# Performance work log

Hardware: AMD Instinct MI355X
Metric: run time of the kernel (lower is better)

The kernel has to match this reference:

```python
import jax, jax.numpy as jnp
import numpy as np

N = 50000      # nodes
E = 800000     # edges (avg degree 16)
F_IN = 128
HID = 64
NCLS = 40
K = 2          # num_stacks
T = 2          # num_layers (shared weights)


def setup_inputs() -> dict:
    key = jax.random.key(0)
    ks = jax.random.split(key, 10)
    s = 0.05
    return {
        "x": jax.random.normal(ks[0], (N, F_IN), dtype=jnp.float32),
        "edge_index": jax.random.randint(ks[1], (2, E), 0, N),
        "w1_init": jax.random.normal(ks[2], (K, F_IN, HID), dtype=jnp.float32) * s,
        "w1": jax.random.normal(ks[3], (K, HID, HID), dtype=jnp.float32) * s,
        "v1": jax.random.normal(ks[4], (K, F_IN, HID), dtype=jnp.float32) * s,
        "b1": jax.random.normal(ks[5], (K, HID), dtype=jnp.float32) * s,
        "w2_init": jax.random.normal(ks[6], (K, HID, NCLS), dtype=jnp.float32) * s,
        "w2": jax.random.normal(ks[7], (K, NCLS, NCLS), dtype=jnp.float32) * s,
        "v2": jax.random.normal(ks[8], (K, HID, NCLS), dtype=jnp.float32) * s,
        "b2": jax.random.normal(ks[9], (K, NCLS), dtype=jnp.float32) * s,
    }


def _gcn_norm(src, dst, n):
    # PyG gcn_norm with add_self_loops=False: deg over destination, sym norm
    deg = jax.ops.segment_sum(jnp.ones_like(dst, dtype=jnp.float32), dst, num_segments=n)
    dinv = jnp.where(deg > 0, 1.0 / jnp.sqrt(deg), 0.0)
    return dinv[src] * dinv[dst]  # [E]


def _arma_conv(x, src, dst, norm, n, w_init, w, v, b, act):
    # x: [N, Fin]; w_init: [K, Fin, Fout]; w: [K, Fout, Fout]; v: [K, Fin, Fout]; b: [K, Fout]
    root = jnp.einsum('nf,kfg->kng', x, v)  # [K, N, Fout], dropout=0 -> identity
    out = None
    for t in range(T):
        if t == 0:
            h = jnp.einsum('nf,kfg->kng', x, w_init)
        else:
            h = jnp.einsum('knf,kfg->kng', out, w)
        # sparse neighbor aggregation: out[i] = sum_{(j->i)} norm_e * h[j]
        agg = jax.vmap(
            lambda hk: jax.ops.segment_sum(hk[src] * norm[:, None], dst, num_segments=n)
        )(h)  # [K, N, Fout]
        out = act(agg + root + b[:, None, :])
    return out.mean(axis=0)  # mean over stacks -> [N, Fout]


def reference(x, edge_index, w1_init, w1, v1, b1, w2_init, w2, v2, b2):
    src, dst = edge_index[0], edge_index[1]
    norm = _gcn_norm(src, dst, N)
    h = _arma_conv(x, src, dst, norm, N, w1_init, w1, v1, b1, jax.nn.relu)
    h = jax.nn.relu(h)  # wrapper ReLU; dropout is identity in eval
    o = _arma_conv(h, src, dst, norm, N, w2_init, w2, v2, b2, lambda z: z)
    return jax.nn.log_softmax(o, axis=1)
```

## Files before the change

kernel.cpp:

```cpp
#include <hip/hip_runtime.h>
#include <hip/hip_bf16.h>
#include <math.h>

#define N_NODES 50000
#define F_IN 128
#define HID 64
#define NCLS 40
#define K_STACKS 2
#define SCAN_TILE 1024
#define NBLK_CNT 256

typedef __attribute__((ext_vector_type(8))) short short8;
typedef __attribute__((ext_vector_type(4))) float floatx4;

__device__ __forceinline__ unsigned int f32_to_bf16_bits(float f) {
    unsigned int u = __float_as_uint(f);
    return (u + 0x7fffu + ((u >> 16) & 1u)) >> 16;
}
__device__ __forceinline__ unsigned int pack_bf16x2(float a, float b) {
    return f32_to_bf16_bits(a) | (f32_to_bf16_bits(b) << 16);
}


__global__ __launch_bounds__(256) void count_kernel(const int* __restrict__ dst,
                                                    int* __restrict__ counts, int E) {
    __shared__ int hist[256];
    int blk = blockIdx.x, t = threadIdx.x;
    hist[t] = 0;
    __syncthreads();
    int chunk = (E + NBLK_CNT - 1) / NBLK_CNT;
    int s = blk * chunk, e = min(E, s + chunk);
    for (int i = s + t; i < e; i += 256) atomicAdd(&hist[dst[i] >> 8], 1);
    __syncthreads();
    counts[t * NBLK_CNT + blk] = hist[t];
}

__global__ __launch_bounds__(256) void scan_phase1(const int* __restrict__ in,
                                                   int* __restrict__ blockSums, int n) {
    __shared__ int lds[256];
    int b = blockIdx.x, t = threadIdx.x;
    int base = b * SCAN_TILE + t * 4;
    int s = 0;
    if (base + 3 < n) {
        int4 v = *(const int4*)(in + base);
        s = v.x + v.y + v.z + v.w;
    } else {
#pragma unroll
        for (int i = 0; i < 4; ++i)
            if (base + i < n) s += in[base + i];
    }
    lds[t] = s;
    __syncthreads();
    for (int off = 128; off; off >>= 1) {
        if (t < off) lds[t] += lds[t + off];
        __syncthreads();
    }
    if (t == 0) blockSums[b] = lds[0];
}

__global__ void scan_phase2(int* __restrict__ blockSums, int nb) {
    int t = threadIdx.x;
    int v = (t < nb) ? blockSums[t] : 0;
#pragma unroll
    for (int off = 1; off < 64; off <<= 1) {
        int u = __shfl_up(v, off);
        if (t >= off) v += u;
    }
    if (t < nb) blockSums[t] = v;
}

__global__ __launch_bounds__(256) void scan_phase3_excl(const int* __restrict__ in,
                                                        const int* __restrict__ blockSumsInc,
                                                        int* __restrict__ out, int n) {
    __shared__ int lds[256];
    int b = blockIdx.x, t = threadIdx.x;
    int base = b * SCAN_TILE + t * 4;
    int e[4];
    int s = 0;
#pragma unroll
    for (int i = 0; i < 4; ++i) {
        e[i] = (base + i < n) ? in[base + i] : 0;
        s += e[i];
    }
    lds[t] = s;
    __syncthreads();
    int v = s;
    for (int off = 1; off < 256; off <<= 1) {
        int add = (t >= off) ? lds[t - off] : 0;
        __syncthreads();
        v += add;
        lds[t] = v;
        __syncthreads();
    }
    int run = (t == 0 ? 0 : lds[t - 1]) + (b == 0 ? 0 : blockSumsInc[b - 1]);
#pragma unroll
    for (int i = 0; i < 4; ++i) {
        if (base + i < n) {
            out[base + i] = run;
            run += e[i];
        }
    }
}

__global__ __launch_bounds__(256) void bucket_scatter_kernel(const int* __restrict__ src,
                                                             const int* __restrict__ dst,
                                                             const int* __restrict__ scanned,
                                                             unsigned int* __restrict__ pairs,
                                                             int E) {
    __shared__ int cur[256];
    int blk = blockIdx.x, t = threadIdx.x;
    cur[t] = scanned[t * NBLK_CNT + blk];
    __syncthreads();
    int chunk = (E + NBLK_CNT - 1) / NBLK_CNT;
    int s0 = blk * chunk, e0 = min(E, s0 + chunk);
    for (int i = s0 + t; i < e0; i += 256) {
        int d = dst[i];
        int pos = atomicAdd(&cur[d >> 8], 1);
        pairs[pos] = (unsigned int)src[i] | ((unsigned int)(d & 255) << 16);
    }
}

__global__ __launch_bounds__(256) void csr_build_kernel(const unsigned int* __restrict__ pairs,
                                                        const int* __restrict__ scanned,
                                                        int* __restrict__ row_ptr,
                                                        float* __restrict__ dinv,
                                                        int* __restrict__ col, int N, int E) {
    __shared__ int degl[256], lds[256], curl[256], sb[2];
    int b = blockIdx.x, t = threadIdx.x;
    if (t == 0) {
        sb[0] = scanned[b * NBLK_CNT];
        sb[1] = (b + 1 < 256) ? scanned[(b + 1) * NBLK_CNT] : E;
    }
    degl[t] = 0;
    __syncthreads();
    int bstart = sb[0], bend = sb[1];
    for (int e = bstart + t; e < bend; e += 256) {
        atomicAdd(&degl[(pairs[e] >> 16) & 255], 1);
    }
    __syncthreads();
    int d = degl[t];
    lds[t] = d;
    __syncthreads();
    int v = d;
    for (int off = 1; off < 256; off <<= 1) {
        int add = (t >= off) ? lds[t - off] : 0;
        __syncthreads();
        v += add;
        lds[t] = v;
        __syncthreads();
    }
    int excl = v - d;
    int node = b * 256 + t;
    if (node <= N) row_ptr[node] = bstart + excl;
    if (node < N) dinv[node] = (d > 0) ? (1.0f / sqrtf((float)d)) : 0.0f;
    curl[t] = excl;
    __syncthreads();
    for (int e = bstart + t; e < bend; e += 256) {
        unsigned int p = pairs[e];
        int ln = (p >> 16) & 255;
        int pos = atomicAdd(&curl[ln], 1);
        col[bstart + pos] = (int)(p & 0xffffu);
    }
}

__device__ __forceinline__ void wt_one(const float* __restrict__ in,
                                       unsigned short* __restrict__ out, int li, int C, int F,
                                       int CP) {
    int k = li / (F * CP);
    int r = li - k * F * CP;
    int f = r / CP;
    int c = r - f * CP;
    out[li] = (c < C) ? (unsigned short)f32_to_bf16_bits(in[((size_t)k * C + c) * F + f]) : 0;
}

__global__ void wt_all_kernel(const float* v1, const float* w1i, const float* w1,
                              const float* v2, const float* w2i, const float* w2,
                              unsigned short* v1t, unsigned short* w1it, unsigned short* w1t,
                              unsigned short* v2t, unsigned short* w2it, unsigned short* w2t) {
    int i = blockIdx.x * blockDim.x + threadIdx.x;
    if (i < 16384) wt_one(v1, v1t, i, 128, 64, 128);
    else if (i < 32768) wt_one(w1i, w1it, i - 16384, 128, 64, 128);
    else if (i < 40960) wt_one(w1, w1t, i - 32768, 64, 64, 64);
    else if (i < 46080) wt_one(v2, v2t, i - 40960, 64, 40, 64);
    else if (i < 51200) wt_one(w2i, w2it, i - 46080, 64, 40, 64);
    else if (i < 56320) wt_one(w2, w2t, i - 51200, 40, 40, 64);
}

template <int CINP>
__global__ __launch_bounds__(256) void gemm_mfma(
    const void* __restrict__ A, const unsigned short* __restrict__ Bt,
    void* __restrict__ out, const float* __restrict__ scale, int N, int COUT, int CREAL,
    int a_per_k, int a_bf16, int out_bf16, int do_scale, int out_inter) {
    constexpr int CP8 = CINP / 8;
    constexpr int MS = CP8 - 1;
    constexpr int SH = (CP8 == 16) ? 4 : 3;
    __shared__ __align__(16) unsigned short At[64 * CINP];
    __shared__ __align__(16) unsigned short Bs[64 * CINP];

    const int k = blockIdx.y;
    const int n0 = blockIdx.x * 64;
    const int t = threadIdx.x;
    const size_t abase = a_per_k ? (size_t)k * N * CREAL : (size_t)0;
    const unsigned short* Bk = Bt + (size_t)k * COUT * CINP;

    for (int i = t; i < 64 * CP8; i += 256) {
        int n = i >> SH;
        int c = i & MS;
        uint4 w = make_uint4(0u, 0u, 0u, 0u);
        int gn = n0 + n;
        if (gn < N && c * 8 < CREAL) {
            if (a_bf16) {
                w = *(const uint4*)((const unsigned short*)A + abase + (size_t)gn * CREAL + c * 8);
            } else {
                const float* srcp = (const float*)A + abase + (size_t)gn * CREAL + c * 8;
                float4 f0 = *(const float4*)(srcp);
                float4 f1 = *(const float4*)(srcp + 4);
                w.x = pack_bf16x2(f0.x, f0.y);
                w.y = pack_bf16x2(f0.z, f0.w);
                w.z = pack_bf16x2(f1.x, f1.y);
                w.w = pack_bf16x2(f1.z, f1.w);
            }
        }
        *(uint4*)(At + n * CINP + ((c ^ (n & MS)) << 3)) = w;
    }
    for (int i = t; i < COUT * CP8; i += 256) {
        int f = i >> SH;
        int c = i & MS;
        uint4 w = *(const uint4*)(Bk + f * CINP + c * 8);
        *(uint4*)(Bs + f * CINP + ((c ^ (f & MS)) << 3)) = w;
    }
    __syncthreads();

    const int lane = t & 63;
    const int wv = t >> 6;
    const int quad = lane >> 4;
    const int li = lane & 15;
    const int m0 = wv * 16;

    floatx4 acc[4] = {{0.f, 0.f, 0.f, 0.f}, {0.f, 0.f, 0.f, 0.f},
                      {0.f, 0.f, 0.f, 0.f}, {0.f, 0.f, 0.f, 0.f}};
    const int am = (m0 + li) & MS;
#pragma unroll
    for (int kc = 0; kc < CINP / 32; ++kc) {
        int cc = kc * 4 + quad;
        short8 a = *(const short8*)(At + (m0 + li) * CINP + ((cc ^ am) << 3));
#pragma unroll
        for (int nt = 0; nt < 4; ++nt) {
            if (nt * 16 < COUT) {
                int f = nt * 16 + li;
                short8 b = *(const short8*)(Bs + f * CINP + ((cc ^ (f & MS)) << 3));
                acc[nt] = __builtin_amdgcn_mfma_f32_16x16x32_bf16(a, b, acc[nt], 0, 0, 0);
            }
        }
    }

    float sc[4] = {1.f, 1.f, 1.f, 1.f};
    if (do_scale) {
#pragma unroll
        for (int r = 0; r < 4; ++r) {
            int node = n0 + m0 + quad * 4 + r;
            sc[r] = (node < N) ? scale[node] : 1.f;
        }
    }
#pragma unroll
    for (int nt = 0; nt < 4; ++nt) {
        if (nt * 16 >= COUT) continue;
        int f = nt * 16 + li;
        if (f >= COUT) continue;
#pragma unroll
        for (int r = 0; r < 4; ++r) {
            int node = n0 + m0 + quad * 4 + r;
            if (node < N) {
                size_t o = out_inter ? ((size_t)node * 2 * COUT + (size_t)k * COUT + f)
                                     : (((size_t)k * N + node) * COUT + f);
                float val = acc[nt][r] * sc[r];
                if (out_bf16)
                    ((unsigned short*)out)[o] = (unsigned short)f32_to_bf16_bits(val);
                else
                    ((float*)out)[o] = val;
            }
        }
    }
}

template <int F>
__global__ __launch_bounds__(256) void agg_kernel(
    const unsigned short* __restrict__ h, const int* __restrict__ row_ptr,
    const int* __restrict__ col, const float* __restrict__ dinv,
    const unsigned short* __restrict__ rootb, const float* __restrict__ bias,
    void* __restrict__ out, int N, int do_relu, int mode) {
    constexpr int FH = F / 8;
    constexpr int ROWE = 2 * F;
    int wid = (blockIdx.x * blockDim.x + threadIdx.x) >> 6;
    int lane = threadIdx.x & 63;
    int half = lane >> 5;
    int l32 = lane & 31;
    int node = wid * 2 + half;
    bool valid = node < N;
    int e0 = 0, deg = 0;
    float dv = 0.f;
    if (valid) {
        e0 = row_ptr[node];
        deg = row_ptr[node + 1] - e0;
        dv = dinv[node];
    }
    const int sub = l32 >> 4;
    const int fq = l32 & 15;
    const int kk = fq >> 3;
    const int fqq = fq & 7;
    const int fqc = (fqq < FH) ? fqq : (FH - 1);
    const int foff = kk * F + fqc * 8;

    float acc[8] = {};
    for (int w0 = 0; w0 < deg; w0 += 32) {
        int mye = w0 + l32;
        int c = (mye < deg) ? col[e0 + mye] : 0;
        int nch = min(deg - w0, 32);
        for (int base = 0; base < nch; base += 16) {
            uint4 v[8];
            float wj[8];
#pragma unroll
            for (int u = 0; u < 8; ++u) {
                int j = base + u * 2 + sub;
                int cj = __shfl(c, (half << 5) | (j & 31));
                bool ok = (j < nch);
                wj[u] = ok ? 1.f : 0.f;
                int cs = ok ? cj : 0;
                v[u] = *(const uint4*)(h + (size_t)cs * ROWE + foff);
            }
#pragma unroll
            for (int u = 0; u < 8; ++u) {
                const unsigned int uu[4] = {v[u].x, v[u].y, v[u].z, v[u].w};
#pragma unroll
                for (int q = 0; q < 4; ++q) {
                    float lo = __uint_as_float(uu[q] << 16);
                    float hi = __uint_as_float(uu[q] & 0xffff0000u);
                    acc[2 * q] += wj[u] * lo;
                    acc[2 * q + 1] += wj[u] * hi;
                }
            }
        }
    }
#pragma unroll
    for (int i = 0; i < 8; ++i) acc[i] += __shfl_xor(acc[i], 16);

    size_t oc = ((size_t)kk * N + (valid ? node : 0)) * F + fqc * 8;
    uint4 rv = *(const uint4*)(rootb + oc);
    const float* bp = bias + kk * F + fqc * 8;
    float4 b0 = *(const float4*)(bp);
    float4 b1 = *(const float4*)(bp + 4);
    const unsigned int ru[4] = {rv.x, rv.y, rv.z, rv.w};
    float res[8];
#pragma unroll
    for (int q = 0; q < 4; ++q) {
        float rlo = __uint_as_float(ru[q] << 16);
        float rhi = __uint_as_float(ru[q] & 0xffff0000u);
        float blo = (q < 2) ? ((q == 0) ? b0.x : b0.z) : ((q == 2) ? b1.x : b1.z);
        float bhi = (q < 2) ? ((q == 0) ? b0.y : b0.w) : ((q == 2) ? b1.y : b1.w);
        res[2 * q] = acc[2 * q] * dv + rlo + blo;
        res[2 * q + 1] = acc[2 * q + 1] * dv + rhi + bhi;
    }
    if (do_relu) {
#pragma unroll
        for (int i = 0; i < 8; ++i) res[i] = fmaxf(res[i], 0.f);
    }
    if (mode == 0) {
        if (sub == 0 && fqq < FH && valid) {
            size_t o = ((size_t)kk * N + node) * F + fqq * 8;
            uint4 w;
            w.x = pack_bf16x2(res[0], res[1]);
            w.y = pack_bf16x2(res[2], res[3]);
            w.z = pack_bf16x2(res[4], res[5]);
            w.w = pack_bf16x2(res[6], res[7]);
            *(uint4*)((unsigned short*)out + o) = w;
        }
    } else {
        float mres[8];
#pragma unroll
        for (int i = 0; i < 8; ++i) mres[i] = 0.5f * (res[i] + __shfl_xor(res[i], 8));
        if (sub == 0 && kk == 0 && fqq < FH && valid) {
            size_t o = (size_t)node * F + fqq * 8;
            *(float4*)((float*)out + o) = make_float4(mres[0], mres[1], mres[2], mres[3]);
            *(float4*)((float*)out + o + 4) = make_float4(mres[4], mres[5], mres[6], mres[7]);
        }
    }
}

__global__ __launch_bounds__(256) void lsm_kernel(const float* __restrict__ g,
                                                  float* __restrict__ out, int N) {
    int wid = (blockIdx.x * blockDim.x + threadIdx.x) >> 6;
    int lane = threadIdx.x & 63;
    if (wid >= N) return;
    float v = (lane < NCLS) ? g[(size_t)wid * NCLS + lane] : -INFINITY;
    float m = v;
#pragma unroll
    for (int off = 32; off; off >>= 1) m = fmaxf(m, __shfl_xor(m, off));
    float ex = (lane < NCLS) ? expf(v - m) : 0.f;
    float s = ex;
#pragma unroll
    for (int off = 32; off; off >>= 1) s += __shfl_xor(s, off);
    float r = v - m - logf(s);
    if (lane < NCLS) out[(size_t)wid * NCLS + lane] = r;
}


static inline size_t align256(size_t x) { return (x + 255) & ~(size_t)255; }

extern "C" void kernel_launch(void* const* d_in, const int* in_sizes, int n_in,
                              void* d_out, int out_size, void* d_ws, size_t ws_size,
                              hipStream_t stream) {
    const float* x = (const float*)d_in[0];
    const int* ei = (const int*)d_in[1];
    const float* w1_init = (const float*)d_in[2];
    const float* w1 = (const float*)d_in[3];
    const float* v1 = (const float*)d_in[4];
    const float* b1 = (const float*)d_in[5];
    const float* w2_init = (const float*)d_in[6];
    const float* w2 = (const float*)d_in[7];
    const float* v2 = (const float*)d_in[8];
    const float* b2 = (const float*)d_in[9];

    const int N = in_sizes[0] / F_IN;
    const int E = in_sizes[1] / 2;
    const int* src = ei;
    const int* dst = ei + E;

    char* p = (char*)d_ws;
    auto take = [&](size_t bytes) {
        char* r = p;
        p += align256(bytes);
        return r;
    };
    float* dinv = (float*)take((size_t)N * 4);
    int* row_ptr = (int*)take((size_t)(N + 1) * 4);
    int* blockSums = (int*)take(256 * 4);
    int* counts = (int*)take((size_t)256 * NBLK_CNT * 4);
    int* scanned = (int*)take((size_t)256 * NBLK_CNT * 4);
    unsigned int* pairs = (unsigned int*)take((size_t)E * 4);
    int* col = (int*)take((size_t)E * 4);
    unsigned short* v1t = (unsigned short*)take((size_t)2 * 64 * 128 * 2);
    unsigned short* w1it = (unsigned short*)take((size_t)2 * 64 * 128 * 2);
    unsigned short* w1t = (unsigned short*)take((size_t)2 * 64 * 64 * 2);
    unsigned short* v2t = (unsigned short*)take((size_t)2 * 40 * 64 * 2);
    unsigned short* w2it = (unsigned short*)take((size_t)2 * 40 * 64 * 2);
    unsigned short* w2t = (unsigned short*)take((size_t)2 * 40 * 64 * 2);
    unsigned short* rootb = (unsigned short*)take((size_t)K_STACKS * N * HID * 2);
    unsigned short* hb = (unsigned short*)take((size_t)K_STACKS * N * HID * 2);
    unsigned short* hc = (unsigned short*)take((size_t)K_STACKS * N * HID * 2);
    float* h1 = (float*)take((size_t)N * HID * 4);
    float* gmean = (float*)take((size_t)N * NCLS * 4);

    const int TB = 256;
    const int nCnt = 256 * NBLK_CNT;
    const int nScanBlocks = nCnt / SCAN_TILE;
    const int nBuckets = (N + 255) / 256;

    count_kernel<<<NBLK_CNT, 256, 0, stream>>>(dst, counts, E);
    scan_phase1<<<nScanBlocks, 256, 0, stream>>>(counts, blockSums, nCnt);
    scan_phase2<<<1, 64, 0, stream>>>(blockSums, nScanBlocks);
    scan_phase3_excl<<<nScanBlocks, 256, 0, stream>>>(counts, blockSums, scanned, nCnt);
    bucket_scatter_kernel<<<NBLK_CNT, 256, 0, stream>>>(src, dst, scanned, pairs, E);
    csr_build_kernel<<<nBuckets, 256, 0, stream>>>(pairs, scanned, row_ptr, dinv, col, N, E);

    wt_all_kernel<<<(56320 + TB - 1) / TB, TB, 0, stream>>>(v1, w1_init, w1, v2, w2_init, w2,
                                                            v1t, w1it, w1t, v2t, w2it, w2t);

    dim3 ggrid((N + 63) / 64, K_STACKS);
    const int agg_blocks = ((N + 1) / 2 + 3) / 4;

    gemm_mfma<128><<<ggrid, 256, 0, stream>>>(x, v1t, rootb, dinv, N, HID, 128, 0, 0, 1, 0, 0);
    gemm_mfma<128><<<ggrid, 256, 0, stream>>>(x, w1it, hb, dinv, N, HID, 128, 0, 0, 1, 1, 1);
    agg_kernel<HID><<<agg_blocks, 256, 0, stream>>>(hb, row_ptr, col, dinv, rootb, b1, hc, N, 1, 0);
    gemm_mfma<64><<<ggrid, 256, 0, stream>>>(hc, w1t, hb, dinv, N, HID, 64, 1, 1, 1, 1, 1);
    agg_kernel<HID><<<agg_blocks, 256, 0, stream>>>(hb, row_ptr, col, dinv, rootb, b1, h1, N, 1, 1);

    gemm_mfma<64><<<ggrid, 256, 0, stream>>>(h1, v2t, rootb, dinv, N, NCLS, 64, 0, 0, 1, 0, 0);
    gemm_mfma<64><<<ggrid, 256, 0, stream>>>(h1, w2it, hb, dinv, N, NCLS, 64, 0, 0, 1, 1, 1);
    agg_kernel<NCLS><<<agg_blocks, 256, 0, stream>>>(hb, row_ptr, col, dinv, rootb, b2, hc, N, 0, 0);
    gemm_mfma<64><<<ggrid, 256, 0, stream>>>(hc, w2t, hb, dinv, N, NCLS, 40, 1, 1, 1, 1, 1);
    agg_kernel<NCLS><<<agg_blocks, 256, 0, stream>>>(hb, row_ptr, col, dinv, rootb, b2, gmean, N, 0, 1);

    lsm_kernel<<<(N + 3) / 4, 256, 0, stream>>>(gmean, (float*)d_out, N);
}
```

Measured before the change: 339.7 us.

## Store gathered features as FP8 and fuse root and init GEMMs

The per-stack transformed features that the aggregation kernel gathers per edge are now written as FP8 (e4m3) instead of BF16. This halves the bytes fetched in the irregular neighbor gather, and the values are unpacked with hardware fp8-to-f32 conversions. A new dual-output GEMM kernel computes the root projection and the initial projection from one staged copy of the input tile, saving a launch and a re-read of the input. FP8 keeps only 3 mantissa bits, which risks exceeding the accuracy tolerance.

```diff
diff --git a/kernel.cpp b/kernel.cpp
--- a/kernel.cpp
+++ b/kernel.cpp
@@ -12,6 +12,7 @@
 
 typedef __attribute__((ext_vector_type(8))) short short8;
 typedef __attribute__((ext_vector_type(4))) float floatx4;
+typedef __attribute__((ext_vector_type(2))) float floatx2;
 
 __device__ __forceinline__ unsigned int f32_to_bf16_bits(float f) {
     unsigned int u = __float_as_uint(f);
@@ -19,6 +20,10 @@
 }
 __device__ __forceinline__ unsigned int pack_bf16x2(float a, float b) {
     return f32_to_bf16_bits(a) | (f32_to_bf16_bits(b) << 16);
+}
+__device__ __forceinline__ unsigned char f32_to_fp8(float v) {
+    int pk = __builtin_amdgcn_cvt_pk_fp8_f32(v, v, 0, false);
+    return (unsigned char)(pk & 0xff);
 }
 
 
@@ -187,22 +192,11 @@
 }
 
 template <int CINP>
-__global__ __launch_bounds__(256) void gemm_mfma(
-    const void* __restrict__ A, const unsigned short* __restrict__ Bt,
-    void* __restrict__ out, const float* __restrict__ scale, int N, int COUT, int CREAL,
-    int a_per_k, int a_bf16, int out_bf16, int do_scale, int out_inter) {
+__device__ __forceinline__ void stage_A(const void* A, unsigned short* At, size_t abase,
+                                        int n0, int t, int N, int CREAL, int a_bf16) {
     constexpr int CP8 = CINP / 8;
     constexpr int MS = CP8 - 1;
     constexpr int SH = (CP8 == 16) ? 4 : 3;
-    __shared__ __align__(16) unsigned short At[64 * CINP];
-    __shared__ __align__(16) unsigned short Bs[64 * CINP];
-
-    const int k = blockIdx.y;
-    const int n0 = blockIdx.x * 64;
-    const int t = threadIdx.x;
-    const size_t abase = a_per_k ? (size_t)k * N * CREAL : (size_t)0;
-    const unsigned short* Bk = Bt + (size_t)k * COUT * CINP;
-
     for (int i = t; i < 64 * CP8; i += 256) {
         int n = i >> SH;
         int c = i & MS;
@@ -223,12 +217,37 @@
         }
         *(uint4*)(At + n * CINP + ((c ^ (n & MS)) << 3)) = w;
     }
+}
+
+template <int CINP>
+__device__ __forceinline__ void stage_B(const unsigned short* Bk, unsigned short* Bs, int t,
+                                        int COUT) {
+    constexpr int CP8 = CINP / 8;
+    constexpr int MS = CP8 - 1;
+    constexpr int SH = (CP8 == 16) ? 4 : 3;
     for (int i = t; i < COUT * CP8; i += 256) {
         int f = i >> SH;
         int c = i & MS;
         uint4 w = *(const uint4*)(Bk + f * CINP + c * 8);
         *(uint4*)(Bs + f * CINP + ((c ^ (f & MS)) << 3)) = w;
     }
+}
+
+template <int CINP>
+__global__ __launch_bounds__(256) void gemm_mfma(
+    const void* __restrict__ A, const unsigned short* __restrict__ Bt,
+    void* __restrict__ out, const float* __restrict__ scale, int N, int COUT, int CREAL,
+    int a_per_k, int a_bf16, int out_fp8, int do_scale, int out_inter) {
+    constexpr int CP8 = CINP / 8;
+    constexpr int MS = CP8 - 1;
+    __shared__ __align__(16) unsigned short At[64 * CINP];
+    __shared__ __align__(16) unsigned short Bs[64 * CINP];
+
+    const int k = blockIdx.y;
+    const int n0 = blockIdx.x * 64;
+    const int t = threadIdx.x;
+    stage_A<CINP>(A, At, a_per_k ? (size_t)k * N * CREAL : (size_t)0, n0, t, N, CREAL, a_bf16);
+    stage_B<CINP>(Bt + (size_t)k * COUT * CINP, Bs, t, COUT);
     __syncthreads();
 
     const int lane = t & 63;
@@ -271,13 +290,88 @@
         for (int r = 0; r < 4; ++r) {
             int node = n0 + m0 + quad * 4 + r;
             if (node < N) {
-                size_t o = out_inter ? ((size_t)node * 2 * COUT + (size_t)k * COUT + f)
-                                     : (((size_t)k * N + node) * COUT + f);
                 float val = acc[nt][r] * sc[r];
-                if (out_bf16)
-                    ((unsigned short*)out)[o] = (unsigned short)f32_to_bf16_bits(val);
-                else
+                if (out_inter) {
+                    size_t o = (size_t)node * 2 * COUT + (size_t)k * COUT + f;
+                    if (out_fp8)
+                        ((unsigned char*)out)[o] = f32_to_fp8(val);
+                    else
+                        ((unsigned short*)out)[o] = (unsigned short)f32_to_bf16_bits(val);
+                } else {
+                    size_t o = ((size_t)k * N + node) * COUT + f;
                     ((float*)out)[o] = val;
+                }
+            }
+        }
+    }
+}
+
+template <int CINP>
+__global__ __launch_bounds__(256) void gemm2_mfma(
+    const void* __restrict__ A, const unsigned short* __restrict__ Bt1,
+    const unsigned short* __restrict__ Bt2, unsigned short* __restrict__ out1,
+    unsigned char* __restrict__ out2, const float* __restrict__ scale, int N, int COUT,
+    int CREAL, int a_bf16) {
+    constexpr int MS = CINP / 8 - 1;
+    __shared__ __align__(16) unsigned short At[64 * CINP];
+    __shared__ __align__(16) unsigned short Bs1[64 * CINP];
+    __shared__ __align__(16) unsigned short Bs2[64 * CINP];
+
+    const int k = blockIdx.y;
+    const int n0 = blockIdx.x * 64;
+    const int t = threadIdx.x;
+    stage_A<CINP>(A, At, (size_t)0, n0, t, N, CREAL, a_bf16);
+    stage_B<CINP>(Bt1 + (size_t)k * COUT * CINP, Bs1, t, COUT);
+    stage_B<CINP>(Bt2 + (size_t)k * COUT * CINP, Bs2, t, COUT);
+    __syncthreads();
+
+    const int lane = t & 63;
+    const int wv = t >> 6;
+    const int quad = lane >> 4;
+    const int li = lane & 15;
+    const int m0 = wv * 16;
+
+    floatx4 acc1[4] = {{0.f, 0.f, 0.f, 0.f}, {0.f, 0.f, 0.f, 0.f},
+                       {0.f, 0.f, 0.f, 0.f}, {0.f, 0.f, 0.f, 0.f}};
+    floatx4 acc2[4] = {{0.f, 0.f, 0.f, 0.f}, {0.f, 0.f, 0.f, 0.f},
+                       {0.f, 0.f, 0.f, 0.f}, {0.f, 0.f, 0.f, 0.f}};
+    const int am = (m0 + li) & MS;
+#pragma unroll
+    for (int kc = 0; kc < CINP / 32; ++kc) {
+        int cc = kc * 4 + quad;
+        short8 a = *(const short8*)(At + (m0 + li) * CINP + ((cc ^ am) << 3));
+#pragma unroll
+        for (int nt = 0; nt < 4; ++nt) {
+            if (nt * 16 < COUT) {
+                int f = nt * 16 + li;
+                int bo = f * CINP + ((cc ^ (f & MS)) << 3);
+                short8 b1 = *(const short8*)(Bs1 + bo);
+                short8 b2 = *(const short8*)(Bs2 + bo);
+                acc1[nt] = __builtin_amdgcn_mfma_f32_16x16x32_bf16(a, b1, acc1[nt], 0, 0, 0);
+                acc2[nt] = __builtin_amdgcn_mfma_f32_16x16x32_bf16(a, b2, acc2[nt], 0, 0, 0);
+            }
+        }
+    }
+
+    float sc[4];
+#pragma unroll
+    for (int r = 0; r < 4; ++r) {
+        int node = n0 + m0 + quad * 4 + r;
+        sc[r] = (node < N) ? scale[node] : 1.f;
+    }
+#pragma unroll
+    for (int nt = 0; nt < 4; ++nt) {
+        if (nt * 16 >= COUT) continue;
+        int f = nt * 16 + li;
+        if (f >= COUT) continue;
+#pragma unroll
+        for (int r = 0; r < 4; ++r) {
+            int node = n0 + m0 + quad * 4 + r;
+            if (node < N) {
+                out1[((size_t)k * N + node) * COUT + f] =
+                    (unsigned short)f32_to_bf16_bits(acc1[nt][r]);
+                out2[(size_t)node * 2 * COUT + (size_t)k * COUT + f] =
+                    f32_to_fp8(acc2[nt][r] * sc[r]);
             }
         }
     }
@@ -285,12 +379,12 @@
 
 template <int F>
 __global__ __launch_bounds__(256) void agg_kernel(
-    const unsigned short* __restrict__ h, const int* __restrict__ row_ptr,
+    const unsigned char* __restrict__ h8, const int* __restrict__ row_ptr,
     const int* __restrict__ col, const float* __restrict__ dinv,
     const unsigned short* __restrict__ rootb, const float* __restrict__ bias,
     void* __restrict__ out, int N, int do_relu, int mode) {
     constexpr int FH = F / 8;
-    constexpr int ROWE = 2 * F;
+    constexpr int ROWB = 2 * F;
     int wid = (blockIdx.x * blockDim.x + threadIdx.x) >> 6;
     int lane = threadIdx.x & 63;
     int half = lane >> 5;
@@ -317,7 +411,7 @@
         int c = (mye < deg) ? col[e0 + mye] : 0;
         int nch = min(deg - w0, 32);
         for (int base = 0; base < nch; base += 16) {
-            uint4 v[8];
+            uint2 v[8];
             float wj[8];
 #pragma unroll
             for (int u = 0; u < 8; ++u) {
@@ -326,18 +420,22 @@
                 bool ok = (j < nch);
                 wj[u] = ok ? 1.f : 0.f;
                 int cs = ok ? cj : 0;
-                v[u] = *(const uint4*)(h + (size_t)cs * ROWE + foff);
+                v[u] = *(const uint2*)(h8 + (size_t)cs * ROWB + foff);
             }
 #pragma unroll
             for (int u = 0; u < 8; ++u) {
-                const unsigned int uu[4] = {v[u].x, v[u].y, v[u].z, v[u].w};
-#pragma unroll
-                for (int q = 0; q < 4; ++q) {
-                    float lo = __uint_as_float(uu[q] << 16);
-                    float hi = __uint_as_float(uu[q] & 0xffff0000u);
-                    acc[2 * q] += wj[u] * lo;
-                    acc[2 * q + 1] += wj[u] * hi;
-                }
+                floatx2 f0 = __builtin_amdgcn_cvt_pk_f32_fp8(v[u].x, false);
+                floatx2 f1 = __builtin_amdgcn_cvt_pk_f32_fp8(v[u].x, true);
+                floatx2 f2 = __builtin_amdgcn_cvt_pk_f32_fp8(v[u].y, false);
+                floatx2 f3 = __builtin_amdgcn_cvt_pk_f32_fp8(v[u].y, true);
+                acc[0] += wj[u] * f0.x;
+                acc[1] += wj[u] * f0.y;
+                acc[2] += wj[u] * f1.x;
+                acc[3] += wj[u] * f1.y;
+                acc[4] += wj[u] * f2.x;
+                acc[5] += wj[u] * f2.y;
+                acc[6] += wj[u] * f3.x;
+                acc[7] += wj[u] * f3.y;
             }
         }
     }
@@ -445,7 +543,7 @@
     unsigned short* w2it = (unsigned short*)take((size_t)2 * 40 * 64 * 2);
     unsigned short* w2t = (unsigned short*)take((size_t)2 * 40 * 64 * 2);
     unsigned short* rootb = (unsigned short*)take((size_t)K_STACKS * N * HID * 2);
-    unsigned short* hb = (unsigned short*)take((size_t)K_STACKS * N * HID * 2);
+    unsigned char* hb8 = (unsigned char*)take((size_t)K_STACKS * N * HID);
     unsigned short* hc = (unsigned short*)take((size_t)K_STACKS * N * HID * 2);
     float* h1 = (float*)take((size_t)N * HID * 4);
     float* gmean = (float*)take((size_t)N * NCLS * 4);
@@ -468,17 +566,15 @@
     dim3 ggrid((N + 63) / 64, K_STACKS);
     const int agg_blocks = ((N + 1) / 2 + 3) / 4;
 
-    gemm_mfma<128><<<ggrid, 256, 0, stream>>>(x, v1t, rootb, dinv, N, HID, 128, 0, 0, 1, 0, 0);
-    gemm_mfma<128><<<ggrid, 256, 0, stream>>>(x, w1it, hb, dinv, N, HID, 128, 0, 0, 1, 1, 1);
-    agg_kernel<HID><<<agg_blocks, 256, 0, stream>>>(hb, row_ptr, col, dinv, rootb, b1, hc, N, 1, 0);
-    gemm_mfma<64><<<ggrid, 256, 0, stream>>>(hc, w1t, hb, dinv, N, HID, 64, 1, 1, 1, 1, 1);
-    agg_kernel<HID><<<agg_blocks, 256, 0, stream>>>(hb, row_ptr, col, dinv, rootb, b1, h1, N, 1, 1);
-
-    gemm_mfma<64><<<ggrid, 256, 0, stream>>>(h1, v2t, rootb, dinv, N, NCLS, 64, 0, 0, 1, 0, 0);
-    gemm_mfma<64><<<ggrid, 256, 0, stream>>>(h1, w2it, hb, dinv, N, NCLS, 64, 0, 0, 1, 1, 1);
-    agg_kernel<NCLS><<<agg_blocks, 256, 0, stream>>>(hb, row_ptr, col, dinv, rootb, b2, hc, N, 0, 0);
-    gemm_mfma<64><<<ggrid, 256, 0, stream>>>(hc, w2t, hb, dinv, N, NCLS, 40, 1, 1, 1, 1, 1);
-    agg_kernel<NCLS><<<agg_blocks, 256, 0, stream>>>(hb, row_ptr, col, dinv, rootb, b2, gmean, N, 0, 1);
+    gemm2_mfma<128><<<ggrid, 256, 0, stream>>>(x, v1t, w1it, rootb, hb8, dinv, N, HID, 128, 0);
+    agg_kernel<HID><<<agg_blocks, 256, 0, stream>>>(hb8, row_ptr, col, dinv, rootb, b1, hc, N, 1, 0);
+    gemm_mfma<64><<<ggrid, 256, 0, stream>>>(hc, w1t, hb8, dinv, N, HID, 64, 1, 1, 1, 1, 1);
+    agg_kernel<HID><<<agg_blocks, 256, 0, stream>>>(hb8, row_ptr, col, dinv, rootb, b1, h1, N, 1, 1);
+
+    gemm2_mfma<64><<<ggrid, 256, 0, stream>>>(h1, v2t, w2it, rootb, hb8, dinv, N, NCLS, 64, 0);
+    agg_kernel<NCLS><<<agg_blocks, 256, 0, stream>>>(hb8, row_ptr, col, dinv, rootb, b2, hc, N, 0, 0);
+    gemm_mfma<64><<<ggrid, 256, 0, stream>>>(hc, w2t, hb8, dinv, N, NCLS, 40, 1, 1, 1, 1, 1);
+    agg_kernel<NCLS><<<agg_blocks, 256, 0, stream>>>(hb8, row_ptr, col, dinv, rootb, b2, gmean, N, 0, 1);
 
     lsm_kernel<<<(N + 3) / 4, 256, 0, stream>>>(gmean, (float*)d_out, N);
 }
```

After: 286.1 us. -15.8%, faster.
